# Optimization experiments

Measured on AMD Instinct MI355X. Metric: run time of the kernel, lower is better.

The kernel has to match this reference:

```python
import jax, jax.numpy as jnp
import numpy as np

V, E, H = 20000, 300, 2400
B, S = 32, 64


def setup_inputs() -> dict:
    key = jax.random.key(0)
    ks = jax.random.split(key, 10)
    s = 0.02
    return {
        "tgt": jax.random.randint(ks[0], (B, S), 0, V),
        "sentence_vec": jax.random.normal(ks[1], (B, H), jnp.float32),
        "embedding": jax.random.normal(ks[2], (V, E), jnp.float32) * s,
        "W_ih": jax.random.normal(ks[3], (3 * H, E), jnp.float32) * s,
        "W_hh": jax.random.normal(ks[4], (3 * H, H), jnp.float32) * s,
        "b_ih": jnp.zeros((3 * H,), jnp.float32),
        "b_hh": jnp.zeros((3 * H,), jnp.float32),
        "W_out": jax.random.normal(ks[5], (V, H), jnp.float32) * s,
        "b_out": jnp.zeros((V,), jnp.float32),
    }


def reference(tgt, sentence_vec, embedding, W_ih, W_hh, b_ih, b_hh, W_out, b_out):
    # Embedding lookup: [B,S,E]
    emb = embedding[tgt]
    # Precompute input-side gate pre-activations for the whole sequence: [B,S,3H]
    x_gates = jnp.einsum("bse,ge->bsg", emb, W_ih) + b_ih

    def step(h, xg):
        # h: [B,H], xg: [B,3H]
        hg = h @ W_hh.T + b_hh
        xr, xz, xn = jnp.split(xg, 3, axis=-1)
        hr, hz, hn = jnp.split(hg, 3, axis=-1)
        r = jax.nn.sigmoid(xr + hr)
        z = jax.nn.sigmoid(xz + hz)
        n = jnp.tanh(xn + r * hn)  # PyTorch GRU: reset applied to (W_hn h + b_hn)
        h_new = (1.0 - z) * n + z * h
        return h_new, h_new

    _, hs = jax.lax.scan(step, sentence_vec, jnp.swapaxes(x_gates, 0, 1))
    out = jnp.swapaxes(hs, 0, 1)  # [B,S,H]
    # Output projection to vocab: [B,S,V]
    return jnp.einsum("bsh,vh->bsv", out, W_out) + b_out
```

## Files before the change

### kernel.cpp

```cpp
#include <hip/hip_runtime.h>
#include <hip/hip_bf16.h>

typedef unsigned short u16;
typedef __attribute__((ext_vector_type(8))) short shortx8;
typedef __attribute__((ext_vector_type(4))) float floatx4;
typedef __attribute__((ext_vector_type(4))) unsigned short ushortx4;

#define B_  32
#define S_  64
#define H_  2400
#define G3_ 7200
#define V_  20000
#define E_  300
#define EP_ 320
#define M_  2048

__device__ __forceinline__ u16 f32_to_bf16_rne(float f) {
  unsigned u = __float_as_uint(f);
  unsigned r = u + 0x7fffu + ((u >> 16) & 1u);
  return (u16)(r >> 16);
}
__device__ __forceinline__ float bf16_to_f32(u16 h) {
  return __uint_as_float(((unsigned)h) << 16);
}
__device__ __forceinline__ void split_bf16(float x, u16& h, u16& l) {
  h = f32_to_bf16_rne(x);
  float rem = x - bf16_to_f32(h);
  l = f32_to_bf16_rne(rem);
}

__device__ __forceinline__ void gl_lds16(const void* g, void* l) {
  __builtin_amdgcn_global_load_lds((const __attribute__((address_space(1))) void*)g,
                                   (__attribute__((address_space(3))) void*)l, 16, 0, 0);
}

__global__ __launch_bounds__(256) void convert_hilo(
    const float* __restrict__ src, int C, int Cp,
    u16* __restrict__ hi, u16* __restrict__ lo) {
  int r = blockIdx.y;
  int c = (blockIdx.x * 256 + threadIdx.x) * 4;
  if (c >= Cp) return;
  float x0, x1, x2, x3;
  if (c + 4 <= C) {
    float4 v = *reinterpret_cast<const float4*>(&src[(size_t)r * C + c]);
    x0 = v.x; x1 = v.y; x2 = v.z; x3 = v.w;
  } else {
    x0 = (c + 0 < C) ? src[(size_t)r * C + c + 0] : 0.f;
    x1 = (c + 1 < C) ? src[(size_t)r * C + c + 1] : 0.f;
    x2 = (c + 2 < C) ? src[(size_t)r * C + c + 2] : 0.f;
    x3 = (c + 3 < C) ? src[(size_t)r * C + c + 3] : 0.f;
  }
  u16 h0,h1,h2,h3,l0,l1,l2,l3;
  split_bf16(x0,h0,l0); split_bf16(x1,h1,l1);
  split_bf16(x2,h2,l2); split_bf16(x3,h3,l3);
  ushortx4 hv = { h0, h1, h2, h3 };
  ushortx4 lv = { l0, l1, l2, l3 };
  *reinterpret_cast<ushortx4*>(&hi[(size_t)r * Cp + c]) = hv;
  *reinterpret_cast<ushortx4*>(&lo[(size_t)r * Cp + c]) = lv;
}

template<bool GATHER>
__global__ __launch_bounds__(256) void gemm3_bf16x3(
    const u16* __restrict__ Ah, const u16* __restrict__ Al,
    const u16* __restrict__ Bh, const u16* __restrict__ Bl,
    const int* __restrict__ gidx,
    const float* __restrict__ bias,
    float* __restrict__ Cc,
    int M, int N, int K) {
  __shared__ __align__(16) u16 sAh[128 * 32];
  __shared__ __align__(16) u16 sAl[128 * 32];
  __shared__ __align__(16) u16 sBh[128 * 32];
  __shared__ __align__(16) u16 sBl[128 * 32];

  const int t = threadIdx.x;
  const int lane = t & 63;
  const int w = t >> 6, wm = w >> 1, wn = w & 1;
  const int m0 = blockIdx.y * 128, n0 = blockIdx.x * 128;

  const int rl = t >> 2;
  const int c8 = (t & 3) * 8;
  size_t aoff0, aoff1;
  {
    int r0 = m0 + rl, r1 = m0 + rl + 64;
    if (GATHER) { r0 = gidx[r0]; r1 = gidx[r1]; }
    aoff0 = (size_t)r0 * K + c8;
    aoff1 = (size_t)r1 * K + c8;
  }
  int nr0 = n0 + rl;       if (nr0 > N - 1) nr0 = N - 1;
  int nr1 = n0 + rl + 64;  if (nr1 > N - 1) nr1 = N - 1;
  size_t boff0 = (size_t)nr0 * K + c8;
  size_t boff1 = (size_t)nr1 * K + c8;

  floatx4 acc[4][4] = {};

  for (int k0 = 0; k0 < K; k0 += 32) {
    __syncthreads();
    gl_lds16(&Ah[aoff0 + k0], (char*)sAh + t * 16);
    gl_lds16(&Ah[aoff1 + k0], (char*)sAh + t * 16 + 4096);
    gl_lds16(&Al[aoff0 + k0], (char*)sAl + t * 16);
    gl_lds16(&Al[aoff1 + k0], (char*)sAl + t * 16 + 4096);
    gl_lds16(&Bh[boff0 + k0], (char*)sBh + t * 16);
    gl_lds16(&Bh[boff1 + k0], (char*)sBh + t * 16 + 4096);
    gl_lds16(&Bl[boff0 + k0], (char*)sBl + t * 16);
    gl_lds16(&Bl[boff1 + k0], (char*)sBl + t * 16 + 4096);
    __syncthreads();

    const int ar = lane & 15, ak = (lane >> 4) * 8;
    shortx8 fah[4], fal[4], fbh[4], fbl[4];
#pragma unroll
    for (int i = 0; i < 4; ++i) {
      int arow = wm * 64 + i * 16 + ar;
      int brow = wn * 64 + i * 16 + ar;
      fah[i] = *reinterpret_cast<const shortx8*>((const char*)sAh + arow * 64 + ak * 2);
      fal[i] = *reinterpret_cast<const shortx8*>((const char*)sAl + arow * 64 + ak * 2);
      fbh[i] = *reinterpret_cast<const shortx8*>((const char*)sBh + brow * 64 + ak * 2);
      fbl[i] = *reinterpret_cast<const shortx8*>((const char*)sBl + brow * 64 + ak * 2);
    }
#pragma unroll
    for (int mi = 0; mi < 4; ++mi)
#pragma unroll
      for (int ni = 0; ni < 4; ++ni) {
        acc[mi][ni] = __builtin_amdgcn_mfma_f32_16x16x32_bf16(fah[mi], fbh[ni], acc[mi][ni], 0, 0, 0);
        acc[mi][ni] = __builtin_amdgcn_mfma_f32_16x16x32_bf16(fah[mi], fbl[ni], acc[mi][ni], 0, 0, 0);
        acc[mi][ni] = __builtin_amdgcn_mfma_f32_16x16x32_bf16(fal[mi], fbh[ni], acc[mi][ni], 0, 0, 0);
      }
  }

#pragma unroll
  for (int mi = 0; mi < 4; ++mi)
#pragma unroll
    for (int ni = 0; ni < 4; ++ni) {
      int col = n0 + wn * 64 + ni * 16 + (lane & 15);
      if (col < N) {
        float bv = bias[col];
        int rowb = m0 + wm * 64 + mi * 16 + (lane >> 4) * 4;
#pragma unroll
        for (int r = 0; r < 4; ++r)
          Cc[(size_t)(rowb + r) * N + col] = acc[mi][ni][r] + bv;
      }
    }
}

__device__ __forceinline__ void gru_epi(
    int b, int s, int j, float ar, float az, float an,
    const float* __restrict__ hprev, int hstride,
    const float* __restrict__ xg, const float* __restrict__ bhh,
    float* __restrict__ hsf, u16* __restrict__ Ahi, u16* __restrict__ Alo) {
  int m = b * S_ + s;
  size_t xb = (size_t)m * G3_;
  float xr = xg[xb + j], xz = xg[xb + H_ + j], xn = xg[xb + 2 * H_ + j];
  float hr = ar + bhh[j], hz = az + bhh[H_ + j], hn = an + bhh[2 * H_ + j];
  float r = 1.f / (1.f + __expf(-(xr + hr)));
  float z = 1.f / (1.f + __expf(-(xz + hz)));
  float n = tanhf(xn + r * hn);
  float hold = hprev[(size_t)b * hstride + j];
  float hnew = (1.f - z) * n + z * hold;
  hsf[(size_t)m * H_ + j] = hnew;
  if (Ahi) {
    u16 hh, ll; split_bf16(hnew, hh, ll);
    Ahi[(size_t)m * H_ + j] = hh;
    Alo[(size_t)m * H_ + j] = ll;
  }
}

__global__ __launch_bounds__(256) void gru_step(
    const float* __restrict__ hprev, int hstride,
    const float* __restrict__ xg, int s,
    const float* __restrict__ Whh, const float* __restrict__ bhh,
    float* __restrict__ hsf, u16* __restrict__ Ahi, u16* __restrict__ Alo) {
  __shared__ __align__(16) float As[32 * 84];
  __shared__ __align__(16) float Wsh[24 * 84];
  const int t = threadIdx.x;
  const int jl = t & 7, b = t >> 3;
  const int j0 = blockIdx.x * 8;
  const int j = j0 + jl;
  float ar = 0.f, az = 0.f, an = 0.f;
  const float* ap  = &As[b * 84];
  const float* wrp = &Wsh[jl * 84];
  const float* wzp = &Wsh[(8 + jl) * 84];
  const float* wnp = &Wsh[(16 + jl) * 84];

  for (int k0 = 0; k0 < H_; k0 += 80) {
    __syncthreads();
    for (int i = t; i < 1120; i += 256) {
      if (i < 640) {
        int row = i / 20, c4 = (i % 20) * 4;
        *reinterpret_cast<float4*>(&As[row * 84 + c4]) =
            *reinterpret_cast<const float4*>(&hprev[(size_t)row * hstride + k0 + c4]);
      } else {
        int ii = i - 640;
        int lr = ii / 20, c4 = (ii % 20) * 4;
        int gate = lr >> 3, jw = lr & 7;
        *reinterpret_cast<float4*>(&Wsh[lr * 84 + c4]) =
            *reinterpret_cast<const float4*>(&Whh[(size_t)(gate * H_ + j0 + jw) * H_ + k0 + c4]);
      }
    }
    __syncthreads();
#pragma unroll 5
    for (int kk = 0; kk < 80; kk += 4) {
      float4 a   = *reinterpret_cast<const float4*>(ap + kk);
      float4 wr4 = *reinterpret_cast<const float4*>(wrp + kk);
      float4 wz4 = *reinterpret_cast<const float4*>(wzp + kk);
      float4 wn4 = *reinterpret_cast<const float4*>(wnp + kk);
      ar += a.x*wr4.x + a.y*wr4.y + a.z*wr4.z + a.w*wr4.w;
      az += a.x*wz4.x + a.y*wz4.y + a.z*wz4.z + a.w*wz4.w;
      an += a.x*wn4.x + a.y*wn4.y + a.z*wn4.z + a.w*wn4.w;
    }
  }
  gru_epi(b, s, j, ar, az, an, hprev, hstride, xg, bhh, hsf, Ahi, Alo);
}

template<bool GATHER>
__global__ __launch_bounds__(256) void gemm_f32_naive(
    const float* __restrict__ A, const int* __restrict__ gidx, int lda,
    const float* __restrict__ Bm, const float* __restrict__ bias,
    float* __restrict__ C, int M, int N, int K) {
  int n = blockIdx.x * 16 + (threadIdx.x & 15);
  int m = blockIdx.y * 16 + (threadIdx.x >> 4);
  if (m >= M || n >= N) return;
  const float* arow = GATHER ? (A + (size_t)gidx[m] * lda) : (A + (size_t)m * lda);
  const float* brow = Bm + (size_t)n * K;
  float acc = 0.f;
  for (int k = 0; k < K; ++k) acc += arow[k] * brow[k];
  C[(size_t)m * N + n] = acc + bias[n];
}

extern "C" void kernel_launch(void* const* d_in, const int* in_sizes, int n_in,
                              void* d_out, int out_size, void* d_ws, size_t ws_size,
                              hipStream_t stream) {
  const int*   tgt  = (const int*)d_in[0];
  const float* sv   = (const float*)d_in[1];
  const float* emb  = (const float*)d_in[2];
  const float* Wih  = (const float*)d_in[3];
  const float* Whh  = (const float*)d_in[4];
  const float* bih  = (const float*)d_in[5];
  const float* bhh  = (const float*)d_in[6];
  const float* Wout = (const float*)d_in[7];
  const float* bout = (const float*)d_in[8];
  float* out = (float*)d_out;
  char* ws = (char*)d_ws;

  size_t off = 0;
  auto alloc = [&](size_t bytes) { size_t o = off; off += (bytes + 255) & ~(size_t)255; return o; };
  size_t o_xg    = alloc((size_t)M_ * G3_ * 4);
  size_t o_hsf   = alloc((size_t)M_ * H_ * 4);
  size_t o_Ahi   = alloc((size_t)M_ * H_ * 2);
  size_t o_Alo   = alloc((size_t)M_ * H_ * 2);
  size_t o_Ehi   = alloc((size_t)V_ * EP_ * 2);
  size_t o_Elo   = alloc((size_t)V_ * EP_ * 2);
  size_t o_WiHi  = alloc((size_t)G3_ * EP_ * 2);
  size_t o_WiLo  = alloc((size_t)G3_ * EP_ * 2);
  size_t o_WoHi  = alloc((size_t)V_ * H_ * 2);
  size_t o_WoLo  = alloc((size_t)V_ * H_ * 2);
  size_t total_needed = off;

  float* xg  = (float*)(ws + o_xg);
  float* hsf = (float*)(ws + o_hsf);

  bool full = (ws_size >= total_needed);

  if (full) {
    u16* Ahi  = (u16*)(ws + o_Ahi);
    u16* Alo  = (u16*)(ws + o_Alo);
    u16* Ehi  = (u16*)(ws + o_Ehi);
    u16* Elo  = (u16*)(ws + o_Elo);
    u16* WiHi = (u16*)(ws + o_WiHi);
    u16* WiLo = (u16*)(ws + o_WiLo);
    u16* WoHi = (u16*)(ws + o_WoHi);
    u16* WoLo = (u16*)(ws + o_WoLo);

    convert_hilo<<<dim3(1, V_),  256, 0, stream>>>(emb,  E_, EP_, Ehi,  Elo);
    convert_hilo<<<dim3(1, G3_), 256, 0, stream>>>(Wih,  E_, EP_, WiHi, WiLo);
    convert_hilo<<<dim3(3, V_),  256, 0, stream>>>(Wout, H_, H_,  WoHi, WoLo);

    gemm3_bf16x3<true><<<dim3(57, 16), 256, 0, stream>>>(
        Ehi, Elo, WiHi, WiLo, tgt, bih, xg, M_, G3_, EP_);

    for (int s = 0; s < S_; ++s) {
      const float* hp = (s == 0) ? sv : (hsf + (size_t)(s - 1) * H_);
      int hstride = (s == 0) ? H_ : S_ * H_;
      gru_step<<<300, 256, 0, stream>>>(hp, hstride, xg, s, Whh, bhh, hsf, Ahi, Alo);
    }

    gemm3_bf16x3<false><<<dim3(157, 16), 256, 0, stream>>>(
        Ahi, Alo, WoHi, WoLo, nullptr, bout, out, M_, V_, H_);
  } else {
    gemm_f32_naive<true><<<dim3(G3_ / 16, M_ / 16), 256, 0, stream>>>(
        emb, tgt, E_, Wih, bih, xg, M_, G3_, E_);
    for (int s = 0; s < S_; ++s) {
      const float* hp = (s == 0) ? sv : (hsf + (size_t)(s - 1) * H_);
      int hstride = (s == 0) ? H_ : S_ * H_;
      gru_step<<<300, 256, 0, stream>>>(hp, hstride, xg, s, Whh, bhh, hsf, nullptr, nullptr);
    }
    gemm_f32_naive<false><<<dim3(V_ / 16, M_ / 16), 256, 0, stream>>>(
        hsf, nullptr, H_, Wout, bout, out, M_, V_, H_);
  }
}
```

Baseline: 7.751 ms.

## Restructure GRU step as split-K direct-load matvec with shared reduction

The per-timestep recurrent kernel drops its LDS-tiled loop over 8 hidden units per block. It now launches 480 blocks of 640 threads, each covering 5 hidden units. Threads read h and W_hh rows directly from global memory over a quarter of K each, and the four partial sums are reduced through shared memory before the epilogue. The aim is more parallelism across the GPU for this latency-bound sequential step, at the cost of uncoalesced per-thread row reads of W_hh and h that depend on caches.

```diff
diff --git a/kernel.cpp b/kernel.cpp
--- a/kernel.cpp
+++ b/kernel.cpp
@@ -163,51 +163,50 @@
   }
 }
 
-__global__ __launch_bounds__(256) void gru_step(
+__global__ __launch_bounds__(640, 5) void gru_step(
     const float* __restrict__ hprev, int hstride,
     const float* __restrict__ xg, int s,
     const float* __restrict__ Whh, const float* __restrict__ bhh,
     float* __restrict__ hsf, u16* __restrict__ Ahi, u16* __restrict__ Alo) {
-  __shared__ __align__(16) float As[32 * 84];
-  __shared__ __align__(16) float Wsh[24 * 84];
+  __shared__ float sR[640], sZ[640], sN[640];
   const int t = threadIdx.x;
-  const int jl = t & 7, b = t >> 3;
-  const int j0 = blockIdx.x * 8;
-  const int j = j0 + jl;
+  const int kq = t / 160;
+  const int r160 = t % 160;
+  const int b = r160 / 5;
+  const int jl = r160 % 5;
+  const int j = blockIdx.x * 5 + jl;
+  const int k0 = kq * 600;
+
+  const float* hp = hprev + (size_t)b * hstride + k0;
+  const float* wr = Whh + (size_t)j * H_ + k0;
+  const float* wz = Whh + (size_t)(H_ + j) * H_ + k0;
+  const float* wn = Whh + (size_t)(2 * H_ + j) * H_ + k0;
   float ar = 0.f, az = 0.f, an = 0.f;
-  const float* ap  = &As[b * 84];
-  const float* wrp = &Wsh[jl * 84];
-  const float* wzp = &Wsh[(8 + jl) * 84];
-  const float* wnp = &Wsh[(16 + jl) * 84];
-
-  for (int k0 = 0; k0 < H_; k0 += 80) {
-    __syncthreads();
-    for (int i = t; i < 1120; i += 256) {
-      if (i < 640) {
-        int row = i / 20, c4 = (i % 20) * 4;
-        *reinterpret_cast<float4*>(&As[row * 84 + c4]) =
-            *reinterpret_cast<const float4*>(&hprev[(size_t)row * hstride + k0 + c4]);
-      } else {
-        int ii = i - 640;
-        int lr = ii / 20, c4 = (ii % 20) * 4;
-        int gate = lr >> 3, jw = lr & 7;
-        *reinterpret_cast<float4*>(&Wsh[lr * 84 + c4]) =
-            *reinterpret_cast<const float4*>(&Whh[(size_t)(gate * H_ + j0 + jw) * H_ + k0 + c4]);
-      }
-    }
-    __syncthreads();
-#pragma unroll 5
-    for (int kk = 0; kk < 80; kk += 4) {
-      float4 a   = *reinterpret_cast<const float4*>(ap + kk);
-      float4 wr4 = *reinterpret_cast<const float4*>(wrp + kk);
-      float4 wz4 = *reinterpret_cast<const float4*>(wzp + kk);
-      float4 wn4 = *reinterpret_cast<const float4*>(wnp + kk);
-      ar += a.x*wr4.x + a.y*wr4.y + a.z*wr4.z + a.w*wr4.w;
-      az += a.x*wz4.x + a.y*wz4.y + a.z*wz4.z + a.w*wz4.w;
-      an += a.x*wn4.x + a.y*wn4.y + a.z*wn4.z + a.w*wn4.w;
-    }
-  }
-  gru_epi(b, s, j, ar, az, an, hprev, hstride, xg, bhh, hsf, Ahi, Alo);
+#pragma unroll 2
+  for (int k = 0; k < 600; k += 8) {
+    float4 a0 = *reinterpret_cast<const float4*>(hp + k);
+    float4 a1 = *reinterpret_cast<const float4*>(hp + k + 4);
+    float4 r0 = *reinterpret_cast<const float4*>(wr + k);
+    float4 r1 = *reinterpret_cast<const float4*>(wr + k + 4);
+    float4 z0 = *reinterpret_cast<const float4*>(wz + k);
+    float4 z1 = *reinterpret_cast<const float4*>(wz + k + 4);
+    float4 n0 = *reinterpret_cast<const float4*>(wn + k);
+    float4 n1 = *reinterpret_cast<const float4*>(wn + k + 4);
+    ar += a0.x*r0.x + a0.y*r0.y + a0.z*r0.z + a0.w*r0.w;
+    az += a0.x*z0.x + a0.y*z0.y + a0.z*z0.z + a0.w*z0.w;
+    an += a0.x*n0.x + a0.y*n0.y + a0.z*n0.z + a0.w*n0.w;
+    ar += a1.x*r1.x + a1.y*r1.y + a1.z*r1.z + a1.w*r1.w;
+    az += a1.x*z1.x + a1.y*z1.y + a1.z*z1.z + a1.w*z1.w;
+    an += a1.x*n1.x + a1.y*n1.y + a1.z*n1.z + a1.w*n1.w;
+  }
+  sR[t] = ar; sZ[t] = az; sN[t] = an;
+  __syncthreads();
+  if (kq == 0) {
+    ar = sR[t] + sR[t + 160] + sR[t + 320] + sR[t + 480];
+    az = sZ[t] + sZ[t + 160] + sZ[t + 320] + sZ[t + 480];
+    an = sN[t] + sN[t + 160] + sN[t + 320] + sN[t + 480];
+    gru_epi(b, s, j, ar, az, an, hprev, hstride, xg, bhh, hsf, Ahi, Alo);
+  }
 }
 
 template<bool GATHER>
@@ -279,7 +278,7 @@
     for (int s = 0; s < S_; ++s) {
       const float* hp = (s == 0) ? sv : (hsf + (size_t)(s - 1) * H_);
       int hstride = (s == 0) ? H_ : S_ * H_;
-      gru_step<<<300, 256, 0, stream>>>(hp, hstride, xg, s, Whh, bhh, hsf, Ahi, Alo);
+      gru_step<<<480, 640, 0, stream>>>(hp, hstride, xg, s, Whh, bhh, hsf, Ahi, Alo);
     }
 
     gemm3_bf16x3<false><<<dim3(157, 16), 256, 0, stream>>>(
@@ -290,7 +289,7 @@
     for (int s = 0; s < S_; ++s) {
       const float* hp = (s == 0) ? sv : (hsf + (size_t)(s - 1) * H_);
       int hstride = (s == 0) ? H_ : S_ * H_;
-      gru_step<<<300, 256, 0, stream>>>(hp, hstride, xg, s, Whh, bhh, hsf, nullptr, nullptr);
+      gru_step<<<480, 640, 0, stream>>>(hp, hstride, xg, s, Whh, bhh, hsf, nullptr, nullptr);
     }
     gemm_f32_naive<false><<<dim3(V_ / 16, M_ / 16), 256, 0, stream>>>(
         hsf, nullptr, H_, Wout, bout, out, M_, V_, H_);
```

After: 19.05 ms. 2.46x slower.
